# Optimization experiments

Measured on AMD Instinct MI355X. Metric: run time of the kernel, lower is better.

The kernel has to match this reference:

```python
import jax, jax.numpy as jnp
import numpy as np

N = 50000   # nodes
E = 800000  # edges (avg degree 16)
IN, H, OUT = 128, 256, 40


def setup_inputs() -> dict:
    key = jax.random.key(0)
    ks = jax.random.split(key, 7)
    x = jax.random.normal(ks[0], (N, IN), dtype=jnp.float32)
    edge_index = jax.random.randint(ks[1], (2, E), 0, N, dtype=jnp.int32)
    def w(k, fi, fo):
        return jax.random.normal(k, (fi, fo), dtype=jnp.float32) / np.sqrt(fi).astype(np.float32)
    return {
        "x": x,
        "edge_index": edge_index,
        "W0": w(ks[2], IN, H), "b0": jnp.zeros((H,), jnp.float32),
        "W1": w(ks[3], H, H),  "b1": jnp.zeros((H,), jnp.float32),
        "W2": w(ks[4], H, H),  "b2": jnp.zeros((H,), jnp.float32),
        "Wh": w(ks[5], H, OUT), "bh": jnp.zeros((OUT,), jnp.float32),
    }


def gcn_conv(x, src, dst, W, b, n):
    """PyG GCNConv: self-loops + symmetric D^-1/2 (A+I) D^-1/2 normalization."""
    h = x @ W  # [N, Fout]
    # degree with self-loop (edge weights are all 1)
    deg = jnp.ones((n,), h.dtype).at[dst].add(1.0)
    inv = jax.lax.rsqrt(deg)  # deg^{-1/2}
    coef = inv[src] * inv[dst]  # [E]
    agg = jax.ops.segment_sum(h[src] * coef[:, None], dst, num_segments=n)
    agg = agg + h * (inv * inv)[:, None]  # self-loop contribution
    return agg + b


def reference(x, edge_index, W0, b0, W1, b1, W2, b2, Wh, bh):
    src, dst = edge_index[0], edge_index[1]
    h = jax.nn.relu(gcn_conv(x, src, dst, W0, b0, N))   # conv0 + relu (dropout p=0)
    h = jax.nn.relu(gcn_conv(h, src, dst, W1, b1, N))   # conv1 + relu
    h = gcn_conv(h, src, dst, W2, b2, N)                # final conv (no relu)
    g = jnp.mean(h, axis=0, keepdims=True)              # batch=None -> global mean, [1, H]
    return g @ Wh + bh                                  # prediction head, [1, OUT]
```

## Files before the change

### kernel.cpp

```cpp
#include <hip/hip_runtime.h>

#define NN 50000
#define NE 800000
#define FIN 128
#define FH 256
#define FOUT 40
#define NPAD 50432
#define NN2 50048
#define NBLK_S 196
#define NB 256
#define BSPAN 196
#define EBLK 4096
#define NBLK_A 196

typedef float f32x4 __attribute__((ext_vector_type(4)));
typedef short bf16x8 __attribute__((ext_vector_type(8)));

__device__ __forceinline__ ushort f2bf(float f) {
    unsigned u = __float_as_uint(f);
    unsigned r = (u + 0x7FFFu + ((u >> 16) & 1u)) >> 16;
    return (ushort)r;
}
__device__ __forceinline__ float bf2f(ushort b) {
    return __uint_as_float(((unsigned)b) << 16);
}


__global__ void cnt_zero_kernel(int* __restrict__ cnt, float* __restrict__ wsum) {
    int i = blockIdx.x * 256 + threadIdx.x;
    if (i < NN) { cnt[i] = 0; wsum[i] = 0.0f; }
}

__global__ void cnt_count_kernel(int* __restrict__ cnt, const int* __restrict__ dst) {
    int e = blockIdx.x * 256 + threadIdx.x;
    if (e < NE) atomicAdd(&cnt[dst[e]], 1);
}

__global__ void inv_kernel(const int* __restrict__ cnt, float* __restrict__ inv) {
    int i = blockIdx.x * 256 + threadIdx.x;
    if (i < NN) inv[i] = rsqrtf((float)(cnt[i] + 1));
}

__global__ __launch_bounds__(256) void bsum_kernel(const int* __restrict__ cnt,
                                                   int* __restrict__ bsum) {
    __shared__ int sh[256];
    int i = blockIdx.x * 256 + threadIdx.x;
    sh[threadIdx.x] = (i < NN) ? cnt[i] : 0;
    __syncthreads();
    #pragma unroll
    for (int off = 128; off > 0; off >>= 1) {
        if (threadIdx.x < off) sh[threadIdx.x] += sh[threadIdx.x + off];
        __syncthreads();
    }
    if (threadIdx.x == 0) bsum[blockIdx.x] = sh[0];
}

__global__ __launch_bounds__(256) void bscan_kernel(int* __restrict__ bsum) {
    __shared__ int sh[256];
    int t = threadIdx.x;
    int v = (t < NBLK_S) ? bsum[t] : 0;
    sh[t] = v;
    __syncthreads();
    #pragma unroll
    for (int off = 1; off < 256; off <<= 1) {
        int u = (t >= off) ? sh[t - off] : 0;
        __syncthreads();
        sh[t] += u;
        __syncthreads();
    }
    if (t < NBLK_S) bsum[t] = sh[t] - v;
}

__global__ __launch_bounds__(256) void emit_kernel(const int* __restrict__ cnt,
                                                   const int* __restrict__ bsum,
                                                   int* __restrict__ row_start) {
    __shared__ int sh[256];
    int i = blockIdx.x * 256 + threadIdx.x;
    int v = (i < NN) ? cnt[i] : 0;
    sh[threadIdx.x] = v;
    __syncthreads();
    #pragma unroll
    for (int off = 1; off < 256; off <<= 1) {
        int u = (threadIdx.x >= off) ? sh[threadIdx.x - off] : 0;
        __syncthreads();
        sh[threadIdx.x] += u;
        __syncthreads();
    }
    int pos = bsum[blockIdx.x] + sh[threadIdx.x] - v;
    if (i <= NN) row_start[i] = pos;
}


__global__ void bcur_init_kernel(const int* __restrict__ row_start, int* __restrict__ bcur) {
    int b = threadIdx.x;
    int n = b * BSPAN; if (n > NN) n = NN;
    bcur[b] = row_start[n];
}

__global__ __launch_bounds__(256) void binA_kernel(const int* __restrict__ src,
                                                   const int* __restrict__ dst,
                                                   int* __restrict__ bcur,
                                                   unsigned* __restrict__ inter) {
    __shared__ int hcnt[NB];
    __shared__ int hoff[NB];
    __shared__ int lcur[NB];
    __shared__ int gbase[NB];
    __shared__ unsigned stage[EBLK];

    const int t  = threadIdx.x;
    const int e0 = blockIdx.x * EBLK;
    const int n  = min(EBLK, NE - e0);

    hcnt[t] = 0;
    __syncthreads();
    for (int i = t; i < n; i += 256)
        atomicAdd(&hcnt[dst[e0 + i] / BSPAN], 1);
    __syncthreads();
    int v = hcnt[t];
    hoff[t] = v;
    __syncthreads();
    #pragma unroll
    for (int off = 1; off < NB; off <<= 1) {
        int u = (t >= off) ? hoff[t - off] : 0;
        __syncthreads();
        hoff[t] += u;
        __syncthreads();
    }
    int excl = hoff[t] - v;
    __syncthreads();
    hoff[t] = excl;
    lcur[t] = excl;
    if (v > 0) gbase[t] = atomicAdd(&bcur[t], v);
    __syncthreads();
    for (int i = t; i < n; i += 256) {
        int d = dst[e0 + i];
        int s = src[e0 + i];
        int b = d / BSPAN;
        int idx = atomicAdd(&lcur[b], 1);
        stage[idx] = ((unsigned)d << 16) | (unsigned)s;
    }
    __syncthreads();
    for (int i = t; i < n; i += 256) {
        unsigned rec = stage[i];
        int b = (int)(rec >> 16) / BSPAN;
        inter[gbase[b] + (i - hoff[b])] = rec;
    }
}

__global__ __launch_bounds__(256) void binB_kernel(const unsigned* __restrict__ inter,
                                                   const int* __restrict__ row_start,
                                                   const float* __restrict__ inv,
                                                   float2* __restrict__ edata,
                                                   float* __restrict__ wsum) {
    __shared__ int lcur[BSPAN];
    const int b   = blockIdx.x;
    const int nlo = b * BSPAN;
    const int nhi = min(nlo + BSPAN, NN);
    const int nn  = nhi - nlo;
    const int base = row_start[nlo];
    const int cnt  = row_start[nhi] - base;
    const int t = threadIdx.x;

    for (int i = t; i < nn; i += 256) lcur[i] = row_start[nlo + i];
    __syncthreads();
    for (int i = t; i < cnt; i += 256) {
        unsigned rec = inter[base + i];
        int d = (int)(rec >> 16);
        int s = (int)(rec & 0xFFFFu);
        float coef = inv[s] * inv[d];
        int pos = atomicAdd(&lcur[d - nlo], 1);
        edata[pos] = make_float2(__int_as_float(s), coef);
        unsafeAtomicAdd(&wsum[s], coef);
    }
}


__global__ void wsplit_kernel(const float* __restrict__ W, int K, int N,
                              ushort* __restrict__ WtH, ushort* __restrict__ WtL) {
    int idx = blockIdx.x * 256 + threadIdx.x;
    if (idx >= K * N) return;
    int n = idx % N;
    int k = idx / N;
    float f = W[idx];
    ushort h = f2bf(f);
    WtH[(size_t)n * K + k] = h;
    if (WtL) WtL[(size_t)n * K + k] = f2bf(f - bf2f(h));
}


template<int TERMS, bool BIAS_RELU>
__global__ __launch_bounds__(256) void gemm_mfma_kernel(
    const ushort* __restrict__ AH, const ushort* __restrict__ AL,
    const ushort* __restrict__ BH, const ushort* __restrict__ BL,
    const float* __restrict__ bias,
    ushort* __restrict__ outB,
    int M, int K) {
    constexpr int NARR = (TERMS == 3) ? 4 : 2;
    __shared__ ushort smem[NARR * 128 * 40];
    ushort* Ah = smem;
    ushort* Bh = smem + 128 * 40;
    ushort* Al = (TERMS == 3) ? smem + 2 * 128 * 40 : nullptr;
    ushort* Bl = (TERMS == 3) ? smem + 3 * 128 * 40 : nullptr;

    const int tid  = threadIdx.x;
    const int lane = tid & 63;
    const int w    = tid >> 6;
    const int wr   = w >> 1;
    const int wc   = w & 1;
    const int row0 = blockIdx.x * 128;
    const int col0 = blockIdx.y * 128;

    f32x4 acc[4][4] = {};

    for (int k0 = 0; k0 < K; k0 += 32) {
        #pragma unroll
        for (int i = 0; i < 2; ++i) {
            int c  = i * 256 + tid;
            int r  = c >> 2;
            int cb = c & 3;
            int gr = row0 + r;
            uint4 vh = make_uint4(0u, 0u, 0u, 0u);
            if (gr < M)
                vh = *reinterpret_cast<const uint4*>(AH + (size_t)gr * K + k0 + cb * 8);
            *reinterpret_cast<uint4*>(&Ah[r * 40 + cb * 8]) = vh;
            *reinterpret_cast<uint4*>(&Bh[r * 40 + cb * 8]) =
                *reinterpret_cast<const uint4*>(BH + (size_t)(col0 + r) * K + k0 + cb * 8);
            if (TERMS == 3) {
                uint4 vl = make_uint4(0u, 0u, 0u, 0u);
                if (gr < M)
                    vl = *reinterpret_cast<const uint4*>(AL + (size_t)gr * K + k0 + cb * 8);
                *reinterpret_cast<uint4*>(&Al[r * 40 + cb * 8]) = vl;
                *reinterpret_cast<uint4*>(&Bl[r * 40 + cb * 8]) =
                    *reinterpret_cast<const uint4*>(BL + (size_t)(col0 + r) * K + k0 + cb * 8);
            }
        }
        __syncthreads();

        const int rsel = lane & 15;
        const int ksel = (lane >> 4) * 8;
        bf16x8 ah[4], bh[4];
        #pragma unroll
        for (int m = 0; m < 4; ++m)
            ah[m] = *reinterpret_cast<const bf16x8*>(&Ah[(wr * 64 + m * 16 + rsel) * 40 + ksel]);
        #pragma unroll
        for (int n = 0; n < 4; ++n)
            bh[n] = *reinterpret_cast<const bf16x8*>(&Bh[(wc * 64 + n * 16 + rsel) * 40 + ksel]);

        if (TERMS == 3) {
            bf16x8 al[4], bl[4];
            #pragma unroll
            for (int m = 0; m < 4; ++m)
                al[m] = *reinterpret_cast<const bf16x8*>(&Al[(wr * 64 + m * 16 + rsel) * 40 + ksel]);
            #pragma unroll
            for (int n = 0; n < 4; ++n)
                bl[n] = *reinterpret_cast<const bf16x8*>(&Bl[(wc * 64 + n * 16 + rsel) * 40 + ksel]);
            #pragma unroll
            for (int m = 0; m < 4; ++m)
                #pragma unroll
                for (int n = 0; n < 4; ++n) {
                    acc[m][n] = __builtin_amdgcn_mfma_f32_16x16x32_bf16(ah[m], bh[n], acc[m][n], 0, 0, 0);
                    acc[m][n] = __builtin_amdgcn_mfma_f32_16x16x32_bf16(ah[m], bl[n], acc[m][n], 0, 0, 0);
                    acc[m][n] = __builtin_amdgcn_mfma_f32_16x16x32_bf16(al[m], bh[n], acc[m][n], 0, 0, 0);
                }
        } else {
            #pragma unroll
            for (int m = 0; m < 4; ++m)
                #pragma unroll
                for (int n = 0; n < 4; ++n)
                    acc[m][n] = __builtin_amdgcn_mfma_f32_16x16x32_bf16(ah[m], bh[n], acc[m][n], 0, 0, 0);
        }
        __syncthreads();
    }

    const int cl = lane & 15;
    const int rg = lane >> 4;
    #pragma unroll
    for (int m = 0; m < 4; ++m) {
        #pragma unroll
        for (int i = 0; i < 4; ++i) {
            int gr = row0 + wr * 64 + m * 16 + rg * 4 + i;
            if (gr < M) {
                #pragma unroll
                for (int n = 0; n < 4; ++n) {
                    int gc = col0 + wc * 64 + n * 16 + cl;
                    float o = acc[m][n][i];
                    if (BIAS_RELU) o = fmaxf(o + bias[gc], 0.0f);
                    outB[(size_t)gr * FH + gc] = f2bf(o);
                }
            }
        }
    }
}


__global__ __launch_bounds__(256) void gather_x_kernel(const float* __restrict__ x,
                                                       const float2* __restrict__ edata,
                                                       const int* __restrict__ row_start,
                                                       const float* __restrict__ inv,
                                                       ushort* __restrict__ outH,
                                                       ushort* __restrict__ outL) {
    int node = blockIdx.x * 4 + (threadIdx.x >> 6);
    int lane = threadIdx.x & 63;
    if (node >= NN) return;

    int beg = row_start[node];
    int end = row_start[node + 1];

    float iv = inv[node];
    float c  = iv * iv;
    float2 v = *reinterpret_cast<const float2*>(x + (size_t)node * FIN + lane * 2);
    float2 a0 = make_float2(v.x * c, v.y * c);
    float2 a1 = make_float2(0.f, 0.f);
    float2 a2 = make_float2(0.f, 0.f);
    float2 a3 = make_float2(0.f, 0.f);

    int i = beg;
    int pre = (4 - (beg & 3)) & 3;
    int pe = beg + pre; if (pe > end) pe = end;
    for (; i < pe; ++i) {
        float2 ed = edata[i];
        float2 w = *reinterpret_cast<const float2*>(x + (size_t)__float_as_int(ed.x) * FIN + lane * 2);
        a0.x += w.x * ed.y; a0.y += w.y * ed.y;
    }
    for (; i + 4 <= end; i += 4) {
        float4 e01 = *reinterpret_cast<const float4*>(&edata[i]);
        float4 e23 = *reinterpret_cast<const float4*>(&edata[i + 2]);
        const float* p0 = x + (size_t)__float_as_int(e01.x) * FIN + lane * 2;
        const float* p1 = x + (size_t)__float_as_int(e01.z) * FIN + lane * 2;
        const float* p2 = x + (size_t)__float_as_int(e23.x) * FIN + lane * 2;
        const float* p3 = x + (size_t)__float_as_int(e23.z) * FIN + lane * 2;
        float2 w0 = *reinterpret_cast<const float2*>(p0);
        float2 w1 = *reinterpret_cast<const float2*>(p1);
        float2 w2 = *reinterpret_cast<const float2*>(p2);
        float2 w3 = *reinterpret_cast<const float2*>(p3);
        a0.x += w0.x * e01.y; a0.y += w0.y * e01.y;
        a1.x += w1.x * e01.w; a1.y += w1.y * e01.w;
        a2.x += w2.x * e23.y; a2.y += w2.y * e23.y;
        a3.x += w3.x * e23.w; a3.y += w3.y * e23.w;
    }
    for (; i < end; ++i) {
        float2 ed = edata[i];
        float2 w = *reinterpret_cast<const float2*>(x + (size_t)__float_as_int(ed.x) * FIN + lane * 2);
        a0.x += w.x * ed.y; a0.y += w.y * ed.y;
    }

    float ax = a0.x + a1.x + a2.x + a3.x;
    float ay = a0.y + a1.y + a2.y + a3.y;
    ushort h0 = f2bf(ax), h1 = f2bf(ay);
    ushort l0 = f2bf(ax - bf2f(h0)), l1 = f2bf(ay - bf2f(h1));
    size_t o = (size_t)node * FIN + lane * 2;
    *reinterpret_cast<ushort2*>(outH + o) = make_ushort2(h0, h1);
    *reinterpret_cast<ushort2*>(outL + o) = make_ushort2(l0, l1);
}


__global__ __launch_bounds__(256) void gather_bf_kernel(const ushort* __restrict__ lin,
                                                        const float2* __restrict__ edata,
                                                        const int* __restrict__ row_start,
                                                        const float* __restrict__ inv,
                                                        const float* __restrict__ bias,
                                                        ushort* __restrict__ outB) {
    int node = blockIdx.x * 4 + (threadIdx.x >> 6);
    int lane = threadIdx.x & 63;
    if (node >= NN) return;

    int beg = row_start[node];
    int end = row_start[node + 1];

    float iv = inv[node];
    float c  = iv * iv;
    ushort4 sv = *reinterpret_cast<const ushort4*>(lin + (size_t)node * FH + lane * 4);
    float4 b = *reinterpret_cast<const float4*>(bias + lane * 4);
    float4 a0 = make_float4(bf2f(sv.x) * c + b.x, bf2f(sv.y) * c + b.y,
                            bf2f(sv.z) * c + b.z, bf2f(sv.w) * c + b.w);
    float4 a1 = make_float4(0.f, 0.f, 0.f, 0.f);
    float4 a2 = make_float4(0.f, 0.f, 0.f, 0.f);
    float4 a3 = make_float4(0.f, 0.f, 0.f, 0.f);

    int i = beg;
    int pre = (4 - (beg & 3)) & 3;
    int pe = beg + pre; if (pe > end) pe = end;
    for (; i < pe; ++i) {
        float2 ed = edata[i];
        float cf = ed.y;
        ushort4 wv = *reinterpret_cast<const ushort4*>(lin + (size_t)__float_as_int(ed.x) * FH + lane * 4);
        a0.x += bf2f(wv.x) * cf; a0.y += bf2f(wv.y) * cf;
        a0.z += bf2f(wv.z) * cf; a0.w += bf2f(wv.w) * cf;
    }
    for (; i + 4 <= end; i += 4) {
        float4 e01 = *reinterpret_cast<const float4*>(&edata[i]);
        float4 e23 = *reinterpret_cast<const float4*>(&edata[i + 2]);
        const ushort* p0 = lin + (size_t)__float_as_int(e01.x) * FH + lane * 4;
        const ushort* p1 = lin + (size_t)__float_as_int(e01.z) * FH + lane * 4;
        const ushort* p2 = lin + (size_t)__float_as_int(e23.x) * FH + lane * 4;
        const ushort* p3 = lin + (size_t)__float_as_int(e23.z) * FH + lane * 4;
        ushort4 w0 = *reinterpret_cast<const ushort4*>(p0);
        ushort4 w1 = *reinterpret_cast<const ushort4*>(p1);
        ushort4 w2 = *reinterpret_cast<const ushort4*>(p2);
        ushort4 w3 = *reinterpret_cast<const ushort4*>(p3);
        a0.x += bf2f(w0.x) * e01.y; a0.y += bf2f(w0.y) * e01.y;
        a0.z += bf2f(w0.z) * e01.y; a0.w += bf2f(w0.w) * e01.y;
        a1.x += bf2f(w1.x) * e01.w; a1.y += bf2f(w1.y) * e01.w;
        a1.z += bf2f(w1.z) * e01.w; a1.w += bf2f(w1.w) * e01.w;
        a2.x += bf2f(w2.x) * e23.y; a2.y += bf2f(w2.y) * e23.y;
        a2.z += bf2f(w2.z) * e23.y; a2.w += bf2f(w2.w) * e23.y;
        a3.x += bf2f(w3.x) * e23.w; a3.y += bf2f(w3.y) * e23.w;
        a3.z += bf2f(w3.z) * e23.w; a3.w += bf2f(w3.w) * e23.w;
    }
    for (; i < end; ++i) {
        float2 ed = edata[i];
        float cf = ed.y;
        ushort4 wv = *reinterpret_cast<const ushort4*>(lin + (size_t)__float_as_int(ed.x) * FH + lane * 4);
        a0.x += bf2f(wv.x) * cf; a0.y += bf2f(wv.y) * cf;
        a0.z += bf2f(wv.z) * cf; a0.w += bf2f(wv.w) * cf;
    }

    float4 acc = make_float4(a0.x + a1.x + a2.x + a3.x,
                             a0.y + a1.y + a2.y + a3.y,
                             a0.z + a1.z + a2.z + a3.z,
                             a0.w + a1.w + a2.w + a3.w);

    float r0 = fmaxf(acc.x, 0.f), r1 = fmaxf(acc.y, 0.f);
    float r2 = fmaxf(acc.z, 0.f), r3 = fmaxf(acc.w, 0.f);
    *reinterpret_cast<ushort4*>(outB + (size_t)node * FH + lane * 4) =
        make_ushort4(f2bf(r0), f2bf(r1), f2bf(r2), f2bf(r3));
}


__global__ void vzero_kernel(float* __restrict__ v) {
    v[threadIdx.x] = 0.0f;
}

__global__ __launch_bounds__(256) void colsumw_kernel(const ushort* __restrict__ a1,
                                                      const float* __restrict__ wsum,
                                                      const float* __restrict__ inv,
                                                      float* __restrict__ v) {
    __shared__ float sh[4][256];
    int wid  = threadIdx.x >> 6;
    int lane = threadIdx.x & 63;
    int r0 = blockIdx.x * 256;
    int r1 = r0 + 256; if (r1 > NN) r1 = NN;

    float4 acc = make_float4(0.f, 0.f, 0.f, 0.f);
    for (int r = r0 + wid; r < r1; r += 4) {
        float iv = inv[r];
        float wr = wsum[r] + iv * iv;
        ushort4 u = *reinterpret_cast<const ushort4*>(a1 + (size_t)r * FH + lane * 4);
        acc.x += bf2f(u.x) * wr;
        acc.y += bf2f(u.y) * wr;
        acc.z += bf2f(u.z) * wr;
        acc.w += bf2f(u.w) * wr;
    }
    *reinterpret_cast<float4*>(&sh[wid][lane * 4]) = acc;
    __syncthreads();
    if (wid == 0) {
        float4 s1 = *reinterpret_cast<const float4*>(&sh[1][lane * 4]);
        float4 s2 = *reinterpret_cast<const float4*>(&sh[2][lane * 4]);
        float4 s3 = *reinterpret_cast<const float4*>(&sh[3][lane * 4]);
        unsafeAtomicAdd(&v[lane * 4 + 0], acc.x + s1.x + s2.x + s3.x);
        unsafeAtomicAdd(&v[lane * 4 + 1], acc.y + s1.y + s2.y + s3.y);
        unsafeAtomicAdd(&v[lane * 4 + 2], acc.z + s1.z + s2.z + s3.z);
        unsafeAtomicAdd(&v[lane * 4 + 3], acc.w + s1.w + s2.w + s3.w);
    }
}

__global__ __launch_bounds__(256) void head2_kernel(const float* __restrict__ v,
                                                    const float* __restrict__ W2,
                                                    const float* __restrict__ b2,
                                                    const float* __restrict__ Wh,
                                                    const float* __restrict__ bh,
                                                    float* __restrict__ out) {
    __shared__ float m[FH];
    int t = threadIdx.x;
    const float scale = 1.0f / (float)NN;
    float s = 0.0f;
    for (int f = 0; f < FH; ++f)
        s += v[f] * W2[f * FH + t];
    m[t] = s * scale + b2[t];
    __syncthreads();
    if (t < FOUT) {
        float o = 0.0f;
        for (int f = 0; f < FH; ++f)
            o += m[f] * Wh[f * FOUT + t];
        out[t] = o + bh[t];
    }
}


extern "C" void kernel_launch(void* const* d_in, const int* in_sizes, int n_in,
                              void* d_out, int out_size, void* d_ws, size_t ws_size,
                              hipStream_t stream) {
    const float* x   = (const float*)d_in[0];
    const int*   ei  = (const int*)d_in[1];
    const float* W0  = (const float*)d_in[2];
    const float* b0  = (const float*)d_in[3];
    const float* W1  = (const float*)d_in[4];
    const float* b1  = (const float*)d_in[5];
    const float* W2  = (const float*)d_in[6];
    const float* b2  = (const float*)d_in[7];
    const float* Wh  = (const float*)d_in[8];
    const float* bh  = (const float*)d_in[9];
    float* out = (float*)d_out;

    const int* src = ei;
    const int* dst = ei + NE;

    float*    inv       = (float*)d_ws;
    int*      cnt       = (int*)(inv + NPAD);
    int*      row_start = cnt + NPAD;
    int*      bsum      = row_start + NPAD;
    int*      bcur      = bsum + 256;
    float*    wsum      = (float*)(bcur + 256);
    unsigned* inter     = (unsigned*)(wsum + NPAD);
    float2*   edata     = (float2*)(inter + NE);
    float*    vbuf      = (float*)(edata + NE);
    ushort*   W0tH      = (ushort*)(vbuf + 256);
    ushort*   W0tL      = W0tH + 256 * 128;
    ushort*   W1tH      = W0tL + 256 * 128;
    ushort*   aggxH     = W1tH + 256 * 256;
    ushort*   aggxL     = aggxH + (size_t)NN2 * 128;
    ushort*   linb      = aggxH;
    ushort*   h0H       = aggxL + (size_t)NN2 * 128;
    ushort*   a1H       = h0H;

    const int nblk_n = (NN + 255) / 256;
    const int nblk_e = (NE + 255) / 256;
    const dim3 gemm_grid((NN + 127) / 128, 2);
    const int nblk_g = (NN + 3) / 4;

    cnt_zero_kernel<<<nblk_n, 256, 0, stream>>>(cnt, wsum);
    cnt_count_kernel<<<nblk_e, 256, 0, stream>>>(cnt, dst);
    inv_kernel<<<nblk_n, 256, 0, stream>>>(cnt, inv);
    bsum_kernel<<<NBLK_S, 256, 0, stream>>>(cnt, bsum);
    bscan_kernel<<<1, 256, 0, stream>>>(bsum);
    emit_kernel<<<NBLK_S, 256, 0, stream>>>(cnt, bsum, row_start);
    bcur_init_kernel<<<1, 256, 0, stream>>>(row_start, bcur);
    binA_kernel<<<NBLK_A, 256, 0, stream>>>(src, dst, bcur, inter);
    binB_kernel<<<NB, 256, 0, stream>>>(inter, row_start, inv, edata, wsum);
    wsplit_kernel<<<(FIN * FH + 255) / 256, 256, 0, stream>>>(W0, FIN, FH, W0tH, W0tL);
    wsplit_kernel<<<(FH * FH + 255) / 256, 256, 0, stream>>>(W1, FH, FH, W1tH, nullptr);

    gather_x_kernel<<<nblk_g, 256, 0, stream>>>(x, edata, row_start, inv, aggxH, aggxL);
    gemm_mfma_kernel<3, true><<<gemm_grid, 256, 0, stream>>>(aggxH, aggxL, W0tH, W0tL, b0,
                                                             h0H, NN, FIN);

    gemm_mfma_kernel<1, false><<<gemm_grid, 256, 0, stream>>>(h0H, nullptr, W1tH, nullptr, nullptr,
                                                              linb, NN, FH);
    gather_bf_kernel<<<nblk_g, 256, 0, stream>>>(linb, edata, row_start, inv, b1, a1H);

    vzero_kernel<<<1, 256, 0, stream>>>(vbuf);
    colsumw_kernel<<<NBLK_S, 256, 0, stream>>>(a1H, wsum, inv, vbuf);
    head2_kernel<<<1, 256, 0, stream>>>(vbuf, W2, b2, Wh, bh, out);
}
```

Measured before the change: 347.5 us.

## Build CSR via bucket counts and per-bucket local scan; unroll gathers by eight

The per-node global atomic degree count and three-kernel scan are replaced with a bucket-level histogram, a single bucket scan, and a per-bucket pass that counts node degrees in shared memory and emits row_start, inv and zeroed wsum. This removes several small kernel launches and the 800K global atomics on node counters. Separately, both gather kernels now unroll the edge loop by eight with pairwise alignment instead of four with four-alignment, to keep more loads in flight at the cost of extra registers. The bucket scan also absorbs the vbuf zeroing, which removes another launch.

```diff
diff --git a/kernel.cpp b/kernel.cpp
--- a/kernel.cpp
+++ b/kernel.cpp
@@ -7,11 +7,11 @@
 #define FOUT 40
 #define NPAD 50432
 #define NN2 50048
-#define NBLK_S 196
 #define NB 256
 #define BSPAN 196
 #define EBLK 4096
 #define NBLK_A 196
+#define NBLK_S 196
 
 typedef float f32x4 __attribute__((ext_vector_type(4)));
 typedef short bf16x8 __attribute__((ext_vector_type(8)));
@@ -26,39 +26,27 @@
 }
 
 
-__global__ void cnt_zero_kernel(int* __restrict__ cnt, float* __restrict__ wsum) {
-    int i = blockIdx.x * 256 + threadIdx.x;
-    if (i < NN) { cnt[i] = 0; wsum[i] = 0.0f; }
-}
-
-__global__ void cnt_count_kernel(int* __restrict__ cnt, const int* __restrict__ dst) {
-    int e = blockIdx.x * 256 + threadIdx.x;
-    if (e < NE) atomicAdd(&cnt[dst[e]], 1);
-}
-
-__global__ void inv_kernel(const int* __restrict__ cnt, float* __restrict__ inv) {
-    int i = blockIdx.x * 256 + threadIdx.x;
-    if (i < NN) inv[i] = rsqrtf((float)(cnt[i] + 1));
-}
-
-__global__ __launch_bounds__(256) void bsum_kernel(const int* __restrict__ cnt,
-                                                   int* __restrict__ bsum) {
-    __shared__ int sh[256];
-    int i = blockIdx.x * 256 + threadIdx.x;
-    sh[threadIdx.x] = (i < NN) ? cnt[i] : 0;
-    __syncthreads();
-    #pragma unroll
-    for (int off = 128; off > 0; off >>= 1) {
-        if (threadIdx.x < off) sh[threadIdx.x] += sh[threadIdx.x + off];
-        __syncthreads();
-    }
-    if (threadIdx.x == 0) bsum[blockIdx.x] = sh[0];
-}
-
-__global__ __launch_bounds__(256) void bscan_kernel(int* __restrict__ bsum) {
+__global__ __launch_bounds__(256) void bucket_cnt_kernel(const int* __restrict__ dst,
+                                                         int* __restrict__ bcnt) {
+    __shared__ int h[NB];
+    const int t = threadIdx.x;
+    h[t] = 0;
+    __syncthreads();
+    const int e0 = blockIdx.x * EBLK;
+    const int n  = min(EBLK, NE - e0);
+    for (int i = t; i < n; i += 256)
+        atomicAdd(&h[dst[e0 + i] / BSPAN], 1);
+    __syncthreads();
+    if (h[t] > 0) atomicAdd(&bcnt[t], h[t]);
+}
+
+__global__ __launch_bounds__(256) void bucket_scan_kernel(const int* __restrict__ bcnt,
+                                                          int* __restrict__ bbase,
+                                                          int* __restrict__ bcur,
+                                                          float* __restrict__ vbuf) {
     __shared__ int sh[256];
     int t = threadIdx.x;
-    int v = (t < NBLK_S) ? bsum[t] : 0;
+    int v = bcnt[t];
     sh[t] = v;
     __syncthreads();
     #pragma unroll
@@ -68,33 +56,11 @@
         sh[t] += u;
         __syncthreads();
     }
-    if (t < NBLK_S) bsum[t] = sh[t] - v;
-}
-
-__global__ __launch_bounds__(256) void emit_kernel(const int* __restrict__ cnt,
-                                                   const int* __restrict__ bsum,
-                                                   int* __restrict__ row_start) {
-    __shared__ int sh[256];
-    int i = blockIdx.x * 256 + threadIdx.x;
-    int v = (i < NN) ? cnt[i] : 0;
-    sh[threadIdx.x] = v;
-    __syncthreads();
-    #pragma unroll
-    for (int off = 1; off < 256; off <<= 1) {
-        int u = (threadIdx.x >= off) ? sh[threadIdx.x - off] : 0;
-        __syncthreads();
-        sh[threadIdx.x] += u;
-        __syncthreads();
-    }
-    int pos = bsum[blockIdx.x] + sh[threadIdx.x] - v;
-    if (i <= NN) row_start[i] = pos;
-}
-
-
-__global__ void bcur_init_kernel(const int* __restrict__ row_start, int* __restrict__ bcur) {
-    int b = threadIdx.x;
-    int n = b * BSPAN; if (n > NN) n = NN;
-    bcur[b] = row_start[n];
+    int excl = sh[t] - v;
+    bbase[t] = excl;
+    bcur[t]  = excl;
+    if (t == 255) bbase[256] = sh[255];
+    vbuf[t] = 0.0f;
 }
 
 __global__ __launch_bounds__(256) void binA_kernel(const int* __restrict__ src,
@@ -147,18 +113,57 @@
     }
 }
 
-__global__ __launch_bounds__(256) void binB_kernel(const unsigned* __restrict__ inter,
-                                                   const int* __restrict__ row_start,
-                                                   const float* __restrict__ inv,
-                                                   float2* __restrict__ edata,
-                                                   float* __restrict__ wsum) {
+__global__ __launch_bounds__(256) void binB1_kernel(const unsigned* __restrict__ inter,
+                                                    const int* __restrict__ bbase,
+                                                    int* __restrict__ row_start,
+                                                    float* __restrict__ inv,
+                                                    float* __restrict__ wsum) {
+    __shared__ int lcnt[BSPAN];
+    __shared__ int sh[256];
+    const int b   = blockIdx.x;
+    const int nlo = b * BSPAN;
+    const int nhi = min(nlo + BSPAN, NN);
+    const int nn  = nhi - nlo;
+    const int base = bbase[b];
+    const int cnt  = bbase[b + 1] - base;
+    const int t = threadIdx.x;
+
+    for (int i = t; i < nn; i += 256) lcnt[i] = 0;
+    __syncthreads();
+    for (int i = t; i < cnt; i += 256)
+        atomicAdd(&lcnt[(int)(inter[base + i] >> 16) - nlo], 1);
+    __syncthreads();
+    int c = (t < nn) ? lcnt[t] : 0;
+    sh[t] = c;
+    __syncthreads();
+    #pragma unroll
+    for (int off = 1; off < 256; off <<= 1) {
+        int u = (t >= off) ? sh[t - off] : 0;
+        __syncthreads();
+        sh[t] += u;
+        __syncthreads();
+    }
+    if (t < nn) {
+        row_start[nlo + t] = base + sh[t] - c;
+        inv[nlo + t]  = rsqrtf((float)(c + 1));
+        wsum[nlo + t] = 0.0f;
+    }
+    if (b == NB - 1 && t == 0) row_start[NN] = NE;
+}
+
+__global__ __launch_bounds__(256) void binB2_kernel(const unsigned* __restrict__ inter,
+                                                    const int* __restrict__ bbase,
+                                                    const int* __restrict__ row_start,
+                                                    const float* __restrict__ inv,
+                                                    float2* __restrict__ edata,
+                                                    float* __restrict__ wsum) {
     __shared__ int lcur[BSPAN];
     const int b   = blockIdx.x;
     const int nlo = b * BSPAN;
     const int nhi = min(nlo + BSPAN, NN);
     const int nn  = nhi - nlo;
-    const int base = row_start[nlo];
-    const int cnt  = row_start[nhi] - base;
+    const int base = bbase[b];
+    const int cnt  = bbase[b + 1] - base;
     const int t = threadIdx.x;
 
     for (int i = t; i < nn; i += 256) lcur[i] = row_start[nlo + i];
@@ -315,30 +320,42 @@
     float2 a3 = make_float2(0.f, 0.f);
 
     int i = beg;
-    int pre = (4 - (beg & 3)) & 3;
-    int pe = beg + pre; if (pe > end) pe = end;
-    for (; i < pe; ++i) {
+    if ((i & 1) && i < end) {
         float2 ed = edata[i];
         float2 w = *reinterpret_cast<const float2*>(x + (size_t)__float_as_int(ed.x) * FIN + lane * 2);
         a0.x += w.x * ed.y; a0.y += w.y * ed.y;
-    }
-    for (; i + 4 <= end; i += 4) {
+        ++i;
+    }
+    for (; i + 8 <= end; i += 8) {
         float4 e01 = *reinterpret_cast<const float4*>(&edata[i]);
         float4 e23 = *reinterpret_cast<const float4*>(&edata[i + 2]);
-        const float* p0 = x + (size_t)__float_as_int(e01.x) * FIN + lane * 2;
-        const float* p1 = x + (size_t)__float_as_int(e01.z) * FIN + lane * 2;
-        const float* p2 = x + (size_t)__float_as_int(e23.x) * FIN + lane * 2;
-        const float* p3 = x + (size_t)__float_as_int(e23.z) * FIN + lane * 2;
-        float2 w0 = *reinterpret_cast<const float2*>(p0);
-        float2 w1 = *reinterpret_cast<const float2*>(p1);
-        float2 w2 = *reinterpret_cast<const float2*>(p2);
-        float2 w3 = *reinterpret_cast<const float2*>(p3);
+        float4 e45 = *reinterpret_cast<const float4*>(&edata[i + 4]);
+        float4 e67 = *reinterpret_cast<const float4*>(&edata[i + 6]);
+        float2 w0 = *reinterpret_cast<const float2*>(x + (size_t)__float_as_int(e01.x) * FIN + lane * 2);
+        float2 w1 = *reinterpret_cast<const float2*>(x + (size_t)__float_as_int(e01.z) * FIN + lane * 2);
+        float2 w2 = *reinterpret_cast<const float2*>(x + (size_t)__float_as_int(e23.x) * FIN + lane * 2);
+        float2 w3 = *reinterpret_cast<const float2*>(x + (size_t)__float_as_int(e23.z) * FIN + lane * 2);
+        float2 w4 = *reinterpret_cast<const float2*>(x + (size_t)__float_as_int(e45.x) * FIN + lane * 2);
+        float2 w5 = *reinterpret_cast<const float2*>(x + (size_t)__float_as_int(e45.z) * FIN + lane * 2);
+        float2 w6 = *reinterpret_cast<const float2*>(x + (size_t)__float_as_int(e67.x) * FIN + lane * 2);
+        float2 w7 = *reinterpret_cast<const float2*>(x + (size_t)__float_as_int(e67.z) * FIN + lane * 2);
         a0.x += w0.x * e01.y; a0.y += w0.y * e01.y;
         a1.x += w1.x * e01.w; a1.y += w1.y * e01.w;
         a2.x += w2.x * e23.y; a2.y += w2.y * e23.y;
         a3.x += w3.x * e23.w; a3.y += w3.y * e23.w;
-    }
-    for (; i < end; ++i) {
+        a0.x += w4.x * e45.y; a0.y += w4.y * e45.y;
+        a1.x += w5.x * e45.w; a1.y += w5.y * e45.w;
+        a2.x += w6.x * e67.y; a2.y += w6.y * e67.y;
+        a3.x += w7.x * e67.w; a3.y += w7.y * e67.w;
+    }
+    for (; i + 2 <= end; i += 2) {
+        float4 e01 = *reinterpret_cast<const float4*>(&edata[i]);
+        float2 w0 = *reinterpret_cast<const float2*>(x + (size_t)__float_as_int(e01.x) * FIN + lane * 2);
+        float2 w1 = *reinterpret_cast<const float2*>(x + (size_t)__float_as_int(e01.z) * FIN + lane * 2);
+        a0.x += w0.x * e01.y; a0.y += w0.y * e01.y;
+        a1.x += w1.x * e01.w; a1.y += w1.y * e01.w;
+    }
+    if (i < end) {
         float2 ed = edata[i];
         float2 w = *reinterpret_cast<const float2*>(x + (size_t)__float_as_int(ed.x) * FIN + lane * 2);
         a0.x += w.x * ed.y; a0.y += w.y * ed.y;
@@ -378,26 +395,27 @@
     float4 a3 = make_float4(0.f, 0.f, 0.f, 0.f);
 
     int i = beg;
-    int pre = (4 - (beg & 3)) & 3;
-    int pe = beg + pre; if (pe > end) pe = end;
-    for (; i < pe; ++i) {
+    if ((i & 1) && i < end) {
         float2 ed = edata[i];
         float cf = ed.y;
         ushort4 wv = *reinterpret_cast<const ushort4*>(lin + (size_t)__float_as_int(ed.x) * FH + lane * 4);
         a0.x += bf2f(wv.x) * cf; a0.y += bf2f(wv.y) * cf;
         a0.z += bf2f(wv.z) * cf; a0.w += bf2f(wv.w) * cf;
-    }
-    for (; i + 4 <= end; i += 4) {
+        ++i;
+    }
+    for (; i + 8 <= end; i += 8) {
         float4 e01 = *reinterpret_cast<const float4*>(&edata[i]);
         float4 e23 = *reinterpret_cast<const float4*>(&edata[i + 2]);
-        const ushort* p0 = lin + (size_t)__float_as_int(e01.x) * FH + lane * 4;
-        const ushort* p1 = lin + (size_t)__float_as_int(e01.z) * FH + lane * 4;
-        const ushort* p2 = lin + (size_t)__float_as_int(e23.x) * FH + lane * 4;
-        const ushort* p3 = lin + (size_t)__float_as_int(e23.z) * FH + lane * 4;
-        ushort4 w0 = *reinterpret_cast<const ushort4*>(p0);
-        ushort4 w1 = *reinterpret_cast<const ushort4*>(p1);
-        ushort4 w2 = *reinterpret_cast<const ushort4*>(p2);
-        ushort4 w3 = *reinterpret_cast<const ushort4*>(p3);
+        float4 e45 = *reinterpret_cast<const float4*>(&edata[i + 4]);
+        float4 e67 = *reinterpret_cast<const float4*>(&edata[i + 6]);
+        ushort4 w0 = *reinterpret_cast<const ushort4*>(lin + (size_t)__float_as_int(e01.x) * FH + lane * 4);
+        ushort4 w1 = *reinterpret_cast<const ushort4*>(lin + (size_t)__float_as_int(e01.z) * FH + lane * 4);
+        ushort4 w2 = *reinterpret_cast<const ushort4*>(lin + (size_t)__float_as_int(e23.x) * FH + lane * 4);
+        ushort4 w3 = *reinterpret_cast<const ushort4*>(lin + (size_t)__float_as_int(e23.z) * FH + lane * 4);
+        ushort4 w4 = *reinterpret_cast<const ushort4*>(lin + (size_t)__float_as_int(e45.x) * FH + lane * 4);
+        ushort4 w5 = *reinterpret_cast<const ushort4*>(lin + (size_t)__float_as_int(e45.z) * FH + lane * 4);
+        ushort4 w6 = *reinterpret_cast<const ushort4*>(lin + (size_t)__float_as_int(e67.x) * FH + lane * 4);
+        ushort4 w7 = *reinterpret_cast<const ushort4*>(lin + (size_t)__float_as_int(e67.z) * FH + lane * 4);
         a0.x += bf2f(w0.x) * e01.y; a0.y += bf2f(w0.y) * e01.y;
         a0.z += bf2f(w0.z) * e01.y; a0.w += bf2f(w0.w) * e01.y;
         a1.x += bf2f(w1.x) * e01.w; a1.y += bf2f(w1.y) * e01.w;
@@ -406,8 +424,25 @@
         a2.z += bf2f(w2.z) * e23.y; a2.w += bf2f(w2.w) * e23.y;
         a3.x += bf2f(w3.x) * e23.w; a3.y += bf2f(w3.y) * e23.w;
         a3.z += bf2f(w3.z) * e23.w; a3.w += bf2f(w3.w) * e23.w;
-    }
-    for (; i < end; ++i) {
+        a0.x += bf2f(w4.x) * e45.y; a0.y += bf2f(w4.y) * e45.y;
+        a0.z += bf2f(w4.z) * e45.y; a0.w += bf2f(w4.w) * e45.y;
+        a1.x += bf2f(w5.x) * e45.w; a1.y += bf2f(w5.y) * e45.w;
+        a1.z += bf2f(w5.z) * e45.w; a1.w += bf2f(w5.w) * e45.w;
+        a2.x += bf2f(w6.x) * e67.y; a2.y += bf2f(w6.y) * e67.y;
+        a2.z += bf2f(w6.z) * e67.y; a2.w += bf2f(w6.w) * e67.y;
+        a3.x += bf2f(w7.x) * e67.w; a3.y += bf2f(w7.y) * e67.w;
+        a3.z += bf2f(w7.z) * e67.w; a3.w += bf2f(w7.w) * e67.w;
+    }
+    for (; i + 2 <= end; i += 2) {
+        float4 e01 = *reinterpret_cast<const float4*>(&edata[i]);
+        ushort4 w0 = *reinterpret_cast<const ushort4*>(lin + (size_t)__float_as_int(e01.x) * FH + lane * 4);
+        ushort4 w1 = *reinterpret_cast<const ushort4*>(lin + (size_t)__float_as_int(e01.z) * FH + lane * 4);
+        a0.x += bf2f(w0.x) * e01.y; a0.y += bf2f(w0.y) * e01.y;
+        a0.z += bf2f(w0.z) * e01.y; a0.w += bf2f(w0.w) * e01.y;
+        a1.x += bf2f(w1.x) * e01.w; a1.y += bf2f(w1.y) * e01.w;
+        a1.z += bf2f(w1.z) * e01.w; a1.w += bf2f(w1.w) * e01.w;
+    }
+    if (i < end) {
         float2 ed = edata[i];
         float cf = ed.y;
         ushort4 wv = *reinterpret_cast<const ushort4*>(lin + (size_t)__float_as_int(ed.x) * FH + lane * 4);
@@ -426,10 +461,6 @@
         make_ushort4(f2bf(r0), f2bf(r1), f2bf(r2), f2bf(r3));
 }
 
-
-__global__ void vzero_kernel(float* __restrict__ v) {
-    v[threadIdx.x] = 0.0f;
-}
 
 __global__ __launch_bounds__(256) void colsumw_kernel(const ushort* __restrict__ a1,
                                                       const float* __restrict__ wsum,
@@ -506,15 +537,15 @@
     const int* dst = ei + NE;
 
     float*    inv       = (float*)d_ws;
-    int*      cnt       = (int*)(inv + NPAD);
-    int*      row_start = cnt + NPAD;
-    int*      bsum      = row_start + NPAD;
-    int*      bcur      = bsum + 256;
-    float*    wsum      = (float*)(bcur + 256);
-    unsigned* inter     = (unsigned*)(wsum + NPAD);
+    int*      row_start = (int*)(inv + NPAD);
+    float*    wsum      = (float*)(row_start + NPAD);
+    int*      bcnt      = (int*)(wsum + NPAD);
+    int*      bbase     = bcnt + 256;
+    int*      bcur      = bbase + 320;
+    float*    vbuf      = (float*)(bcur + 256);
+    unsigned* inter     = (unsigned*)(vbuf + 256);
     float2*   edata     = (float2*)(inter + NE);
-    float*    vbuf      = (float*)(edata + NE);
-    ushort*   W0tH      = (ushort*)(vbuf + 256);
+    ushort*   W0tH      = (ushort*)(edata + NE);
     ushort*   W0tL      = W0tH + 256 * 128;
     ushort*   W1tH      = W0tL + 256 * 128;
     ushort*   aggxH     = W1tH + 256 * 256;
@@ -523,20 +554,15 @@
     ushort*   h0H       = aggxL + (size_t)NN2 * 128;
     ushort*   a1H       = h0H;
 
-    const int nblk_n = (NN + 255) / 256;
-    const int nblk_e = (NE + 255) / 256;
     const dim3 gemm_grid((NN + 127) / 128, 2);
     const int nblk_g = (NN + 3) / 4;
 
-    cnt_zero_kernel<<<nblk_n, 256, 0, stream>>>(cnt, wsum);
-    cnt_count_kernel<<<nblk_e, 256, 0, stream>>>(cnt, dst);
-    inv_kernel<<<nblk_n, 256, 0, stream>>>(cnt, inv);
-    bsum_kernel<<<NBLK_S, 256, 0, stream>>>(cnt, bsum);
-    bscan_kernel<<<1, 256, 0, stream>>>(bsum);
-    emit_kernel<<<NBLK_S, 256, 0, stream>>>(cnt, bsum, row_start);
-    bcur_init_kernel<<<1, 256, 0, stream>>>(row_start, bcur);
+    hipMemsetAsync(bcnt, 0, NB * sizeof(int), stream);
+    bucket_cnt_kernel<<<NBLK_A, 256, 0, stream>>>(dst, bcnt);
+    bucket_scan_kernel<<<1, 256, 0, stream>>>(bcnt, bbase, bcur, vbuf);
     binA_kernel<<<NBLK_A, 256, 0, stream>>>(src, dst, bcur, inter);
-    binB_kernel<<<NB, 256, 0, stream>>>(inter, row_start, inv, edata, wsum);
+    binB1_kernel<<<NB, 256, 0, stream>>>(inter, bbase, row_start, inv, wsum);
+    binB2_kernel<<<NB, 256, 0, stream>>>(inter, bbase, row_start, inv, edata, wsum);
     wsplit_kernel<<<(FIN * FH + 255) / 256, 256, 0, stream>>>(W0, FIN, FH, W0tH, W0tL);
     wsplit_kernel<<<(FH * FH + 255) / 256, 256, 0, stream>>>(W1, FH, FH, W1tH, nullptr);
 
@@ -548,7 +574,6 @@
                                                               linb, NN, FH);
     gather_bf_kernel<<<nblk_g, 256, 0, stream>>>(linb, edata, row_start, inv, b1, a1H);
 
-    vzero_kernel<<<1, 256, 0, stream>>>(vbuf);
     colsumw_kernel<<<NBLK_S, 256, 0, stream>>>(a1H, wsum, inv, vbuf);
     head2_kernel<<<1, 256, 0, stream>>>(vbuf, W2, b2, Wh, bh, out);
 }
```

Result: faster. 314.9 us (-9.4%).
